# Performance work log

Hardware: AMD Instinct MI355X
Metric: run time of the kernel (lower is better)

## Reference

```python
import jax, jax.numpy as jnp
import numpy as np

H = 1024          # hidden_size
I = 4 * H         # intermediate_size
E = 8             # num routed experts
TOP_K = 2


def setup_inputs() -> dict:
    key = jax.random.key(0)
    ks = jax.random.split(key, 6)
    s = 0.02
    hidden_states = jax.random.normal(ks[0], (4, 4096, H), dtype=jnp.float32)
    # shared expert (num_shared_experts = 1)
    w1_shared = jax.random.normal(ks[1], (H, I), dtype=jnp.float32) * s  # up proj
    w2_shared = jax.random.normal(ks[2], (I, H), dtype=jnp.float32) * s  # down proj
    # routed experts stacked
    w1_routed = jax.random.normal(ks[3], (E, H, I), dtype=jnp.float32) * s
    w2_routed = jax.random.normal(ks[4], (E, I, H), dtype=jnp.float32) * s
    w_router = jax.random.normal(ks[5], (H, E), dtype=jnp.float32) * s
    return {
        "hidden_states": hidden_states,
        "w1_shared": w1_shared,
        "w2_shared": w2_shared,
        "w1_routed": w1_routed,
        "w2_routed": w2_routed,
        "w_router": w_router,
    }


def reference(hidden_states, w1_shared, w2_shared, w1_routed, w2_routed, w_router):
    bsz, seq_len, hidden_dim = hidden_states.shape
    flat = hidden_states.reshape(-1, hidden_dim)              # [T, H]

    # shared expert(s)
    shared_out = jax.nn.silu(flat @ w1_shared) @ w2_shared     # [T, H]

    # router -> softmax -> top-k -> renormalize
    router_logits = flat @ w_router                            # [T, E]
    routing_weights = jax.nn.softmax(router_logits, axis=-1)
    topk_w, topk_idx = jax.lax.top_k(routing_weights, TOP_K)   # [T, K]
    topk_w = topk_w / jnp.sum(topk_w, axis=-1, keepdims=True)

    # combine weights per expert: cw[t, e] = sum_k topk_w[t,k] * (topk_idx[t,k] == e)
    one_hot = jax.nn.one_hot(topk_idx, E, dtype=topk_w.dtype)  # [T, K, E]
    cw = jnp.einsum('tk,tke->te', topk_w, one_hot)             # [T, E]

    # per-expert dense MLP, weighted combine (zero weight == not routed)
    routed_out = jnp.zeros_like(flat)
    for e in range(E):  # fixed small loop over experts
        expert_out = jax.nn.silu(flat @ w1_routed[e]) @ w2_routed[e]  # [T, H]
        routed_out = routed_out + cw[:, e:e + 1] * expert_out

    total = shared_out + routed_out
    return total.reshape(bsz, seq_len, hidden_dim)
```

## Files before the change

### kernel.cpp

```cpp
#include <hip/hip_runtime.h>
#include <cmath>

typedef __bf16 bf16;
typedef bf16 bf16x4 __attribute__((ext_vector_type(4)));
typedef bf16 bf16x8 __attribute__((ext_vector_type(8)));
typedef float f32x4 __attribute__((ext_vector_type(4)));

#define T_TOK 16384
#define HD 1024
#define ID 4096
#define MAXR 51200

__device__ __forceinline__ void async16(const void* g, void* l) {
  void* gp = (void*)g;
  __builtin_amdgcn_global_load_lds((__attribute__((address_space(1))) void*)gp,
                                   (__attribute__((address_space(3))) void*)l,
                                   16, 0, 0);
}

__global__ __launch_bounds__(1024)
void cast_router_kernel(const float* __restrict__ X, const float* __restrict__ Wr,
                        bf16* __restrict__ Xb, int* __restrict__ topk_idx,
                        float* __restrict__ topk_w) {
  __shared__ float W[1024 * 9];
  for (int i = threadIdx.x; i < 1024 * 8; i += 1024)
    W[(i >> 3) * 9 + (i & 7)] = Wr[i];
  __syncthreads();
  const int wave = threadIdx.x >> 6, lane = threadIdx.x & 63;
  const int t = blockIdx.x * 16 + wave;
  const float* xr = X + (size_t)t * HD;
  bf16* xb = Xb + (size_t)t * HD;
  float acc[8] = {0.f, 0.f, 0.f, 0.f, 0.f, 0.f, 0.f, 0.f};
#pragma unroll
  for (int j = 0; j < 4; ++j) {
    const int base = lane * 4 + j * 256;
    const float4 v = *(const float4*)(xr + base);
    bf16x4 o;
    o.x = (bf16)v.x; o.y = (bf16)v.y; o.z = (bf16)v.z; o.w = (bf16)v.w;
    *(bf16x4*)(xb + base) = o;
    const float xv[4] = {v.x, v.y, v.z, v.w};
#pragma unroll
    for (int c = 0; c < 4; ++c) {
      const float* wp = &W[(base + c) * 9];
#pragma unroll
      for (int e2 = 0; e2 < 8; ++e2) acc[e2] += xv[c] * wp[e2];
    }
  }
#pragma unroll
  for (int off = 32; off; off >>= 1)
#pragma unroll
    for (int e2 = 0; e2 < 8; ++e2) acc[e2] += __shfl_down(acc[e2], off);
  if (lane == 0) {
    int i0 = 0; float m0 = acc[0];
#pragma unroll
    for (int e2 = 1; e2 < 8; ++e2) if (acc[e2] > m0) { m0 = acc[e2]; i0 = e2; }
    int i1 = -1; float m1 = -3.4e38f;
#pragma unroll
    for (int e2 = 0; e2 < 8; ++e2)
      if (e2 != i0 && acc[e2] > m1) { m1 = acc[e2]; i1 = e2; }
    const float w0 = 1.f / (1.f + __expf(m1 - m0));
    topk_idx[2 * t] = i0;  topk_idx[2 * t + 1] = i1;
    topk_w[2 * t] = w0;    topk_w[2 * t + 1] = 1.f - w0;
  }
}

__global__ __launch_bounds__(256)
void transpose_cast(const float* __restrict__ srcR, const float* __restrict__ srcS,
                    bf16* __restrict__ dst, int R, int C) {
  const int e = blockIdx.z;
  const float* src = (e < 8) ? srcR + (size_t)e * R * C : srcS;
  __shared__ float tile[64][65];
  const int c0 = blockIdx.x * 64, r0 = blockIdx.y * 64;
  const int tx = threadIdx.x & 15;
  const int ty = threadIdx.x >> 4;
#pragma unroll
  for (int i = 0; i < 64; i += 16) {
    const float4 v = *(const float4*)(src + (size_t)(r0 + ty + i) * C + c0 + tx * 4);
    tile[ty + i][tx * 4 + 0] = v.x;
    tile[ty + i][tx * 4 + 1] = v.y;
    tile[ty + i][tx * 4 + 2] = v.z;
    tile[ty + i][tx * 4 + 3] = v.w;
  }
  __syncthreads();
  bf16* d = dst + (size_t)e * R * C;
#pragma unroll
  for (int i = 0; i < 64; i += 16) {
    const int col = ty + i;
    bf16x4 o;
    o.x = (bf16)tile[tx * 4 + 0][col];
    o.y = (bf16)tile[tx * 4 + 1][col];
    o.z = (bf16)tile[tx * 4 + 2][col];
    o.w = (bf16)tile[tx * 4 + 3][col];
    *(bf16x4*)(d + (size_t)(c0 + col) * R + r0 + tx * 4) = o;
  }
}

__global__ __launch_bounds__(1024)
void scatter_kernel(const int* __restrict__ topk_idx, const float* __restrict__ topk_w,
                    int* __restrict__ row_token, float* __restrict__ row_w,
                    int* __restrict__ row_exp, int* __restrict__ token_rows,
                    int* __restrict__ meta) {
  const int e = blockIdx.x;
  const int tid = threadIdx.x;
  const int wv = tid >> 6, ln = tid & 63;
  __shared__ int whist[16][8];
  __shared__ int hist[8];

  int lc0 = 0, lc1 = 0, lc2 = 0, lc3 = 0, lc4 = 0, lc5 = 0, lc6 = 0, lc7 = 0;
  for (int t = tid; t < T_TOK; t += 1024) {
    const int i0 = topk_idx[2 * t], i1 = topk_idx[2 * t + 1];
    lc0 += (i0 == 0) + (i1 == 0);  lc1 += (i0 == 1) + (i1 == 1);
    lc2 += (i0 == 2) + (i1 == 2);  lc3 += (i0 == 3) + (i1 == 3);
    lc4 += (i0 == 4) + (i1 == 4);  lc5 += (i0 == 5) + (i1 == 5);
    lc6 += (i0 == 6) + (i1 == 6);  lc7 += (i0 == 7) + (i1 == 7);
  }
#pragma unroll
  for (int off = 32; off; off >>= 1) {
    lc0 += __shfl_down(lc0, off); lc1 += __shfl_down(lc1, off);
    lc2 += __shfl_down(lc2, off); lc3 += __shfl_down(lc3, off);
    lc4 += __shfl_down(lc4, off); lc5 += __shfl_down(lc5, off);
    lc6 += __shfl_down(lc6, off); lc7 += __shfl_down(lc7, off);
  }
  if (ln == 0) {
    whist[wv][0] = lc0; whist[wv][1] = lc1; whist[wv][2] = lc2; whist[wv][3] = lc3;
    whist[wv][4] = lc4; whist[wv][5] = lc5; whist[wv][6] = lc6; whist[wv][7] = lc7;
  }
  __syncthreads();
  if (tid < 8) {
    int s = 0;
#pragma unroll
    for (int w = 0; w < 16; ++w) s += whist[w][tid];
    hist[tid] = s;
  }
  __syncthreads();

  if (e == 8) {
    for (int r = tid; r < T_TOK; r += 1024) {
      row_token[r] = r; row_w[r] = 1.f; row_exp[r] = 8;
    }
    if (tid == 0) {
      int tot = T_TOK;
      for (int i = 0; i < 8; ++i) tot += (hist[i] + 255) & ~255;
      meta[0] = tot;
    }
    return;
  }

  int base = T_TOK;
  for (int i = 0; i < e; ++i) base += (hist[i] + 255) & ~255;
  const int cnt = hist[e];
  const int pc = (cnt + 255) & ~255;

  __shared__ int wsum[16];
  int written = 0;
  for (int c = 0; c < T_TOK / 1024; ++c) {
    const int t = c * 1024 + tid;
    const int i0 = topk_idx[2 * t], i1 = topk_idx[2 * t + 1];
    const int slot = (i0 == e) ? 0 : ((i1 == e) ? 1 : -1);
    const unsigned long long m = __ballot(slot >= 0);
    if (ln == 0) wsum[wv] = (int)__popcll(m);
    __syncthreads();
    int off = written;
    for (int i = 0; i < wv; ++i) off += wsum[i];
    if (slot >= 0) {
      const int rank = (int)__popcll(m & ((1ULL << ln) - 1ULL));
      const int pos = base + off + rank;
      row_token[pos] = t;
      row_w[pos] = topk_w[2 * t + slot];
      row_exp[pos] = e;
      token_rows[2 * t + slot] = pos;
    }
    int tot = 0;
#pragma unroll
    for (int i = 0; i < 16; ++i) tot += wsum[i];
    written += tot;
    __syncthreads();
  }
  for (int p = written + tid; p < pc; p += 1024) {
    row_token[base + p] = 0; row_w[base + p] = 0.f; row_exp[base + p] = e;
  }
}

template <int MODE, int NDIM, int KDIM>
__global__ __launch_bounds__(512)
void gemm8(const bf16* __restrict__ A0, const bf16* __restrict__ WT,
           bf16* __restrict__ bout, float* __restrict__ out,
           const int* __restrict__ row_token, const float* __restrict__ row_w,
           const int* __restrict__ row_exp, const int* __restrict__ meta,
           int range_start, int chunk_base) {
  constexpr int NT = KDIM / 32;
  const int total = meta[0];

  const int gx = gridDim.x;
  const int nwg = gx * gridDim.y;
  int id = blockIdx.y * gx + blockIdx.x;
  {
    const int q = nwg >> 3, rm = nwg & 7;
    const int xcd = id & 7, loc = id >> 3;
    id = (xcd < rm ? xcd * (q + 1) : rm * (q + 1) + (xcd - rm) * q) + loc;
  }
  const int bx = id % gx, by = id / gx;

  const int r0 = range_start + by * 256;
  if (r0 >= total) return;
  const int n0 = bx * 256;

  __shared__ __align__(16) char lds[3 * 32768];

  const int tid = threadIdx.x;
  const int wid = tid >> 6, lane = tid & 63;
  const int e = row_exp[r0];
  const bf16* W = WT + (size_t)e * NDIM * KDIM;

  const int tr = tid >> 2;
  const int tb = tid & 3;
  const int rA0 = tr, rA1 = tr + 128;
  const int bl0 = tb ^ ((rA0 >> 1) & 3);
  const int bl1 = tb ^ ((rA1 >> 1) & 3);
  const bf16 *gA0, *gA1;
  if (MODE == 0) {
    gA0 = A0 + (size_t)row_token[r0 + rA0] * KDIM + bl0 * 8;
    gA1 = A0 + (size_t)row_token[r0 + rA1] * KDIM + bl1 * 8;
  } else {
    gA0 = A0 + (size_t)(r0 - chunk_base + rA0) * KDIM + bl0 * 8;
    gA1 = A0 + (size_t)(r0 - chunk_base + rA1) * KDIM + bl1 * 8;
  }
  const bf16* gB0 = W + (size_t)(n0 + rA0) * KDIM + bl0 * 8;
  const bf16* gB1 = W + (size_t)(n0 + rA1) * KDIM + bl1 * 8;
  char* const ldsb = lds;
  const int wo = wid * 1024;

#define STAGE_A0(c, kt) async16(gA0 + (kt) * 32, ldsb + (c) * 32768 + wo)
#define STAGE_A1(c, kt) async16(gA1 + (kt) * 32, ldsb + (c) * 32768 + 8192 + wo)
#define STAGE_B0(c, kt) async16(gB0 + (kt) * 32, ldsb + (c) * 32768 + 16384 + wo)
#define STAGE_B1(c, kt) async16(gB1 + (kt) * 32, ldsb + (c) * 32768 + 24576 + wo)

  const int l15 = lane & 15, kg = lane >> 4;
  const int wr = wid >> 2, wc = wid & 3;
  int offA[8], offB[4];
#pragma unroll
  for (int m = 0; m < 8; ++m) {
    const int row = wr * 128 + m * 16 + l15;
    offA[m] = row * 64 + ((kg ^ ((row >> 1) & 3)) << 4);
  }
#pragma unroll
  for (int n = 0; n < 4; ++n) {
    const int row = wc * 64 + n * 16 + l15;
    offB[n] = 16384 + row * 64 + ((kg ^ ((row >> 1) & 3)) << 4);
  }

  f32x4 acc[8][4] = {};

  STAGE_A0(0, 0); STAGE_A1(0, 0); STAGE_B0(0, 0); STAGE_B1(0, 0);
  STAGE_A0(1, 1); STAGE_A1(1, 1); STAGE_B0(1, 1); STAGE_B1(1, 1);

  int cb = 0, cn = 2;
  for (int kt = 0; kt < NT; ++kt) {
    if (kt + 1 < NT) asm volatile("s_waitcnt vmcnt(4)" ::: "memory");
    else             asm volatile("s_waitcnt vmcnt(0)" ::: "memory");
    __builtin_amdgcn_s_barrier();
    asm volatile("" ::: "memory");
    __builtin_amdgcn_sched_barrier(0);
    const char* Tb = ldsb + cb * 32768;
    const bool pf = (kt + 2 < NT);
    const int k2 = kt + 2;
    bf16x8 bfr[4];
#pragma unroll
    for (int q = 0; q < 4; ++q) {
      if (pf) {
        if (q == 0)      STAGE_A0(cn, k2);
        else if (q == 1) STAGE_A1(cn, k2);
        else if (q == 2) STAGE_B0(cn, k2);
        else             STAGE_B1(cn, k2);
      }
      if (q == 0) {
#pragma unroll
        for (int n = 0; n < 4; ++n) bfr[n] = *(const bf16x8*)(Tb + offB[n]);
      }
      const bf16x8 a0 = *(const bf16x8*)(Tb + offA[2 * q]);
      const bf16x8 a1 = *(const bf16x8*)(Tb + offA[2 * q + 1]);
      __builtin_amdgcn_s_setprio(1);
#pragma unroll
      for (int n = 0; n < 4; ++n) {
        acc[2 * q][n] =
            __builtin_amdgcn_mfma_f32_16x16x32_bf16(a0, bfr[n], acc[2 * q][n], 0, 0, 0);
        acc[2 * q + 1][n] =
            __builtin_amdgcn_mfma_f32_16x16x32_bf16(a1, bfr[n], acc[2 * q + 1][n], 0, 0, 0);
      }
      __builtin_amdgcn_s_setprio(0);
    }
    cb = (cb == 2) ? 0 : cb + 1;
    cn = (cn == 2) ? 0 : cn + 1;
  }
#undef STAGE_A0
#undef STAGE_A1
#undef STAGE_B0
#undef STAGE_B1

  const int orow = wr * 128;
  const int ocol = n0 + wc * 64;
  if (MODE == 0) {
#pragma unroll
    for (int m = 0; m < 8; ++m) {
#pragma unroll
      for (int rr = 0; rr < 4; ++rr) {
        const int row = (r0 - chunk_base) + orow + m * 16 + kg * 4 + rr;
        bf16* p = bout + (size_t)row * NDIM + ocol + l15;
#pragma unroll
        for (int n = 0; n < 4; ++n) {
          const float x = acc[m][n][rr];
          __builtin_nontemporal_store((bf16)(x / (1.f + __expf(-x))), &p[n * 16]);
        }
      }
    }
  } else if (e == 8) {
#pragma unroll
    for (int m = 0; m < 8; ++m) {
#pragma unroll
      for (int rr = 0; rr < 4; ++rr) {
        const int row = r0 + orow + m * 16 + kg * 4 + rr;
        const int tok = row_token[row];
        float* p = out + (size_t)tok * HD + ocol + l15;
#pragma unroll
        for (int n = 0; n < 4; ++n) p[n * 16] = acc[m][n][rr];
      }
    }
  } else {
#pragma unroll
    for (int m = 0; m < 8; ++m) {
#pragma unroll
      for (int rr = 0; rr < 4; ++rr) {
        const int row = r0 + orow + m * 16 + kg * 4 + rr;
        const float w = row_w[row];
        bf16* p = bout + (size_t)(row - T_TOK) * HD + ocol + l15;
#pragma unroll
        for (int n = 0; n < 4; ++n)
          __builtin_nontemporal_store((bf16)(w * acc[m][n][rr]), &p[n * 16]);
      }
    }
  }
}

__global__ __launch_bounds__(256)
void combine_kernel(float* __restrict__ out, const bf16* __restrict__ routed_out,
                    const int* __restrict__ token_rows) {
  const int t = blockIdx.x;
  const int i = threadIdx.x * 4;
  const int rA = token_rows[2 * t] - T_TOK;
  const int rB = token_rows[2 * t + 1] - T_TOK;
  float4 o = *(const float4*)(out + (size_t)t * HD + i);
  const bf16x4 a = *(const bf16x4*)(routed_out + (size_t)rA * HD + i);
  const bf16x4 b = *(const bf16x4*)(routed_out + (size_t)rB * HD + i);
  o.x += (float)a.x + (float)b.x;
  o.y += (float)a.y + (float)b.y;
  o.z += (float)a.z + (float)b.z;
  o.w += (float)a.w + (float)b.w;
  *(float4*)(out + (size_t)t * HD + i) = o;
}

extern "C" void kernel_launch(void* const* d_in, const int* in_sizes, int n_in,
                              void* d_out, int out_size, void* d_ws, size_t ws_size,
                              hipStream_t stream) {
  const float* X   = (const float*)d_in[0];
  const float* w1s = (const float*)d_in[1];
  const float* w2s = (const float*)d_in[2];
  const float* w1r = (const float*)d_in[3];
  const float* w2r = (const float*)d_in[4];
  const float* wr  = (const float*)d_in[5];
  float* out = (float*)d_out;

  char* ws = (char*)d_ws;
  bf16* W1T       = (bf16*)(ws + 0);
  bf16* W2T       = (bf16*)(ws + 75497472);
  bf16* Xbf       = (bf16*)(ws + 150994944);
  int* topk_idx   = (int*)(ws + 184549376);
  float* topk_w   = (float*)(ws + 184680448);
  int* row_token  = (int*)(ws + 184811520);
  float* row_w    = (float*)(ws + 185016320);
  int* row_exp    = (int*)(ws + 185221120);
  int* token_rows = (int*)(ws + 185425920);
  int* meta       = (int*)(ws + 185556992);
  bf16* routed_out= (bf16*)(ws + 185557248);
  bf16* act       = (bf16*)(ws + 256860416);

  const size_t avail = ws_size - 256860416ULL;
  long long rc = (long long)(avail / (ID * 2));
  if (rc > MAXR) rc = MAXR;
  rc &= ~255LL;
  if (rc < 256) rc = 256;
  const int Rc = (int)rc;

  cast_router_kernel<<<T_TOK / 16, 1024, 0, stream>>>(X, wr, Xbf, topk_idx, topk_w);
  transpose_cast<<<dim3(ID / 64, HD / 64, 9), 256, 0, stream>>>(w1r, w1s, W1T, HD, ID);
  transpose_cast<<<dim3(HD / 64, ID / 64, 9), 256, 0, stream>>>(w2r, w2s, W2T, ID, HD);
  scatter_kernel<<<9, 1024, 0, stream>>>(topk_idx, topk_w, row_token, row_w,
                                         row_exp, token_rows, meta);

  for (int cb = 0; cb < MAXR; cb += Rc) {
    const int ce = (cb + Rc < MAXR) ? cb + Rc : MAXR;
    gemm8<0, ID, HD><<<dim3(ID / 256, (ce - cb) / 256), 512, 0, stream>>>(
        Xbf, W1T, act, nullptr, row_token, row_w, row_exp, meta, cb, cb);
    gemm8<1, HD, ID><<<dim3(HD / 256, (ce - cb) / 256), 512, 0, stream>>>(
        act, W2T, routed_out, out, row_token, row_w, row_exp, meta, cb, cb);
  }
  combine_kernel<<<T_TOK, 256, 0, stream>>>(out, routed_out, token_rows);
}
```

Before: 1.235 ms.

## Restructure GEMM main loop into two barrier-separated phases with batched fragment loads

Splits each k-tile iteration into two halves. Each half loads all its A/B fragments from LDS up front, issues half of the next-tile prefetch, synchronizes, and then runs a block of 16 MFMAs. The vmcnt wait moves to the second half, with an initial wait before the loop. This aims to overlap global prefetch and LDS reads with MFMA work in a ping-pong style schedule, at the cost of extra barriers per iteration. It also replaces the nontemporal stores in the bf16 epilogues with plain stores, so intermediate results can stay in cache for the next GEMM.

Measured after the change: 1.255 ms. Within noise of the previous version (+1.6%).

```diff
diff --git a/kernel.cpp b/kernel.cpp
--- a/kernel.cpp
+++ b/kernel.cpp
@@ -253,42 +253,50 @@
 
   STAGE_A0(0, 0); STAGE_A1(0, 0); STAGE_B0(0, 0); STAGE_B1(0, 0);
   STAGE_A0(1, 1); STAGE_A1(1, 1); STAGE_B0(1, 1); STAGE_B1(1, 1);
+  asm volatile("s_waitcnt vmcnt(4)" ::: "memory");
+  __builtin_amdgcn_s_barrier();
 
   int cb = 0, cn = 2;
   for (int kt = 0; kt < NT; ++kt) {
-    if (kt + 1 < NT) asm volatile("s_waitcnt vmcnt(4)" ::: "memory");
-    else             asm volatile("s_waitcnt vmcnt(0)" ::: "memory");
-    __builtin_amdgcn_s_barrier();
-    asm volatile("" ::: "memory");
-    __builtin_amdgcn_sched_barrier(0);
     const char* Tb = ldsb + cb * 32768;
     const bool pf = (kt + 2 < NT);
     const int k2 = kt + 2;
-    bf16x8 bfr[4];
-#pragma unroll
-    for (int q = 0; q < 4; ++q) {
-      if (pf) {
-        if (q == 0)      STAGE_A0(cn, k2);
-        else if (q == 1) STAGE_A1(cn, k2);
-        else if (q == 2) STAGE_B0(cn, k2);
-        else             STAGE_B1(cn, k2);
-      }
-      if (q == 0) {
-#pragma unroll
-        for (int n = 0; n < 4; ++n) bfr[n] = *(const bf16x8*)(Tb + offB[n]);
-      }
-      const bf16x8 a0 = *(const bf16x8*)(Tb + offA[2 * q]);
-      const bf16x8 a1 = *(const bf16x8*)(Tb + offA[2 * q + 1]);
-      __builtin_amdgcn_s_setprio(1);
-#pragma unroll
-      for (int n = 0; n < 4; ++n) {
-        acc[2 * q][n] =
-            __builtin_amdgcn_mfma_f32_16x16x32_bf16(a0, bfr[n], acc[2 * q][n], 0, 0, 0);
-        acc[2 * q + 1][n] =
-            __builtin_amdgcn_mfma_f32_16x16x32_bf16(a1, bfr[n], acc[2 * q + 1][n], 0, 0, 0);
-      }
-      __builtin_amdgcn_s_setprio(0);
-    }
+    bf16x8 bfr[4], afr[4];
+
+#pragma unroll
+    for (int n = 0; n < 4; ++n) bfr[n] = *(const bf16x8*)(Tb + offB[n]);
+#pragma unroll
+    for (int m = 0; m < 4; ++m) afr[m] = *(const bf16x8*)(Tb + offA[m]);
+    if (pf) { STAGE_A0(cn, k2); STAGE_A1(cn, k2); }
+    __builtin_amdgcn_s_barrier();
+    asm volatile("s_waitcnt lgkmcnt(0)" ::: "memory");
+    __builtin_amdgcn_sched_barrier(0);
+    __builtin_amdgcn_s_setprio(1);
+#pragma unroll
+    for (int m = 0; m < 4; ++m)
+#pragma unroll
+      for (int n = 0; n < 4; ++n)
+        acc[m][n] = __builtin_amdgcn_mfma_f32_16x16x32_bf16(afr[m], bfr[n], acc[m][n], 0, 0, 0);
+    __builtin_amdgcn_s_setprio(0);
+    __builtin_amdgcn_s_barrier();
+
+#pragma unroll
+    for (int m = 0; m < 4; ++m) afr[m] = *(const bf16x8*)(Tb + offA[4 + m]);
+    if (pf) { STAGE_B0(cn, k2); STAGE_B1(cn, k2); }
+    if (kt + 2 < NT)      asm volatile("s_waitcnt vmcnt(4)" ::: "memory");
+    else if (kt + 1 < NT) asm volatile("s_waitcnt vmcnt(0)" ::: "memory");
+    __builtin_amdgcn_s_barrier();
+    asm volatile("s_waitcnt lgkmcnt(0)" ::: "memory");
+    __builtin_amdgcn_sched_barrier(0);
+    __builtin_amdgcn_s_setprio(1);
+#pragma unroll
+    for (int m = 0; m < 4; ++m)
+#pragma unroll
+      for (int n = 0; n < 4; ++n)
+        acc[4 + m][n] = __builtin_amdgcn_mfma_f32_16x16x32_bf16(afr[m], bfr[n], acc[4 + m][n], 0, 0, 0);
+    __builtin_amdgcn_s_setprio(0);
+    __builtin_amdgcn_s_barrier();
+
     cb = (cb == 2) ? 0 : cb + 1;
     cn = (cn == 2) ? 0 : cn + 1;
   }
@@ -309,7 +317,7 @@
 #pragma unroll
         for (int n = 0; n < 4; ++n) {
           const float x = acc[m][n][rr];
-          __builtin_nontemporal_store((bf16)(x / (1.f + __expf(-x))), &p[n * 16]);
+          p[n * 16] = (bf16)(x / (1.f + __expf(-x)));
         }
       }
     }
@@ -334,8 +342,7 @@
         const float w = row_w[row];
         bf16* p = bout + (size_t)(row - T_TOK) * HD + ocol + l15;
 #pragma unroll
-        for (int n = 0; n < 4; ++n)
-          __builtin_nontemporal_store((bf16)(w * acc[m][n][rr]), &p[n * 16]);
+        for (int n = 0; n < 4; ++n) p[n * 16] = (bf16)(w * acc[m][n][rr]);
       }
     }
   }
```
